# Kernel optimization log

Hardware: AMD Instinct MI355X
Metric: run time of the kernel (lower is better)

Reference implementation:

```python
import jax, jax.numpy as jnp
import numpy as np

EMBED_DIM = 1024
NUM_HEADS = 16
HEAD_DIM = EMBED_DIM // NUM_HEADS
BOARD = 32
SEQ = BOARD * BOARD
BATCH = 16


def setup_inputs() -> dict:
    key = jax.random.key(0)
    ks = jax.random.split(key, 6)
    x = jax.random.normal(ks[0], (BATCH, SEQ, EMBED_DIM), dtype=jnp.float32)
    scale = 1.0 / np.sqrt(EMBED_DIM)
    Wq = jax.random.normal(ks[1], (EMBED_DIM, EMBED_DIM), dtype=jnp.float32) * scale
    Wk = jax.random.normal(ks[2], (EMBED_DIM, EMBED_DIM), dtype=jnp.float32) * scale
    Wv = jax.random.normal(ks[3], (EMBED_DIM, EMBED_DIM), dtype=jnp.float32) * scale
    Wo = jax.random.normal(ks[4], (EMBED_DIM, EMBED_DIM), dtype=jnp.float32) * scale
    rel_bias = jax.random.normal(ks[5], (NUM_HEADS, 2 * BOARD - 1), dtype=jnp.float32)
    return {"x": x, "Wq": Wq, "Wk": Wk, "Wv": Wv, "Wo": Wo, "rel_bias": rel_bias}


def _rel_indices():
    # coords of the flattened H*W grid
    idx = jnp.arange(SEQ)
    rows = idx // BOARD
    cols = idx % BOARD
    offset = BOARD - 1
    rel_x = cols[None, :] - cols[:, None] + offset  # [S, S]
    rel_y = rows[None, :] - rows[:, None] + offset  # [S, S]
    return rel_x, rel_y


def reference(x, Wq, Wk, Wv, Wo, rel_bias):
    B, S, E = x.shape
    H, D = NUM_HEADS, HEAD_DIM
    # projections (Linear with bias=False: x @ W.T; weights here stored as [E, E] applied as x @ W)
    q = (x @ Wq).reshape(B, S, H, D).transpose(0, 2, 1, 3)  # [B,H,S,D]
    k = (x @ Wk).reshape(B, S, H, D).transpose(0, 2, 1, 3)
    v = (x @ Wv).reshape(B, S, H, D).transpose(0, 2, 1, 3)
    scores = jnp.einsum('bhqd,bhkd->bhqk', q, k) / jnp.sqrt(jnp.float32(D))
    rel_x, rel_y = _rel_indices()
    bias = rel_bias[:, rel_x] + rel_bias[:, rel_y]  # [H, S, S]
    scores = scores + bias[None]
    attn = jax.nn.softmax(scores, axis=-1)
    out = jnp.einsum('bhqk,bhkd->bhqd', attn, v)
    out = out.transpose(0, 2, 1, 3).reshape(B, S, E)
    return out @ Wo
```

## Files before the change

### kernel.cpp

```cpp
#include <hip/hip_runtime.h>

#define SEQ   1024
#define EMBED 1024
#define NH    16
#define HD    64
#define NB    16

typedef float facc4 __attribute__((ext_vector_type(4)));
typedef float facc16 __attribute__((ext_vector_type(16)));
typedef short frag8 __attribute__((ext_vector_type(8)));
typedef short sv4 __attribute__((ext_vector_type(4)));

__device__ __forceinline__ unsigned short f2bf(float f) {
  union { float f; unsigned int u; } c; c.f = f;
  unsigned int u = c.u;
  u += 0x7FFFu + ((u >> 16) & 1u);
  return (unsigned short)(u >> 16);
}

__device__ __forceinline__ unsigned int pk_bf16(float lo, float hi) {
  unsigned int r;
  asm("v_cvt_pk_bf16_f32 %0, %1, %2" : "=v"(r) : "v"(lo), "v"(hi));
  return r;
}

__device__ __forceinline__ void gl_lds16(const void* g, void* l) {
  __builtin_amdgcn_global_load_lds(
      (const __attribute__((address_space(1))) unsigned int*)g,
      (__attribute__((address_space(3))) unsigned int*)l, 16, 0, 0);
}

__global__ __launch_bounds__(256) void convert_x_kernel(
    const float* __restrict__ x, unsigned short* __restrict__ xb, int n8) {
  int stride = gridDim.x * blockDim.x;
  for (int i = blockIdx.x * blockDim.x + threadIdx.x; i < n8; i += stride) {
    const float4* src = (const float4*)(x + (size_t)i * 8);
    float4 v0 = src[0], v1 = src[1];
    frag8 o;
    o[0] = f2bf(v0.x); o[1] = f2bf(v0.y); o[2] = f2bf(v0.z); o[3] = f2bf(v0.w);
    o[4] = f2bf(v1.x); o[5] = f2bf(v1.y); o[6] = f2bf(v1.z); o[7] = f2bf(v1.w);
    *(frag8*)(xb + (size_t)i * 8) = o;
  }
}

__global__ __launch_bounds__(256) void transpose_w_kernel(
    const float* W0, const float* W1, const float* W2, const float* W3,
    unsigned short* T0, unsigned short* T1, unsigned short* T2, unsigned short* T3) {
  __shared__ float tw[64][65];
  const float* W; unsigned short* T;
  switch (blockIdx.z) {
    case 0: W = W0; T = T0; break;
    case 1: W = W1; T = T1; break;
    case 2: W = W2; T = T2; break;
    default: W = W3; T = T3; break;
  }
  int k0 = blockIdx.y * 64, n0 = blockIdx.x * 64;
  int t = threadIdx.x;
#pragma unroll
  for (int rep = 0; rep < 4; ++rep) {
    int c = rep * 256 + t;
    int row = c >> 4, ch = c & 15;
    float4 v = *(const float4*)(W + (size_t)(k0 + row) * 1024 + n0 + ch * 4);
    tw[row][ch * 4 + 0] = v.x; tw[row][ch * 4 + 1] = v.y;
    tw[row][ch * 4 + 2] = v.z; tw[row][ch * 4 + 3] = v.w;
  }
  __syncthreads();
#pragma unroll
  for (int rep = 0; rep < 2; ++rep) {
    int c = rep * 256 + t;
    int nrow = c >> 3, ch = c & 7;
    frag8 o;
#pragma unroll
    for (int i = 0; i < 8; ++i) o[i] = (short)f2bf(tw[ch * 8 + i][nrow]);
    *(frag8*)(T + (size_t)(n0 + nrow) * 1024 + k0 + ch * 8) = o;
  }
}

template <int MODE>
__global__ __launch_bounds__(512, 2) void gemm256(
    const unsigned short* __restrict__ A, const unsigned short* __restrict__ Bt,
    unsigned short* __restrict__ qo, unsigned short* __restrict__ ko,
    unsigned short* __restrict__ vto, float* __restrict__ fo, int N) {
  __shared__ unsigned short a_s[2][256 * 64];
  __shared__ unsigned short b_s[2][256 * 64];
  const int tid = threadIdx.x;
  const int w = tid >> 6, l = tid & 63;
  const int l15 = l & 15, l4 = l >> 4;
  const int wr = w >> 2, wc = w & 3;

  const int bid = blockIdx.x;
  const int xcd = bid & 7, j = bid >> 3;
  const int mt = xcd * 8 + (j & 7), nt = j >> 3;
  const int m0 = mt << 8, n0 = nt << 8;

  const int ldrow = l >> 3;
  const int swz8 = ((l & 7) ^ (ldrow & 7)) << 3;
  const unsigned short* Ab = A + (size_t)m0 * 1024;
  const unsigned short* Bb = Bt + (size_t)n0 * 1024;

  facc4 acc[8][4];
#pragma unroll
  for (int mi = 0; mi < 8; ++mi)
#pragma unroll
    for (int nj = 0; nj < 4; ++nj)
#pragma unroll
      for (int r = 0; r < 4; ++r) acc[mi][nj][r] = 0.f;

  auto STAGE_A = [&](int buf, int half, int kt) {
#pragma unroll
    for (int i = 0; i < 2; ++i) {
      const int c = (w << 1) + i;
      const int rb = (half << 7) + (c << 3);
      gl_lds16(Ab + (size_t)kt * 64 + (size_t)(rb + ldrow) * 1024 + swz8,
               &a_s[buf][rb << 6]);
    }
  };
  auto STAGE_B = [&](int buf, int half, int kt) {
#pragma unroll
    for (int i = 0; i < 2; ++i) {
      const int c = (w << 1) + i;
      const int rb = (half << 7) + (c << 3);
      gl_lds16(Bb + (size_t)kt * 64 + (size_t)(rb + ldrow) * 1024 + swz8,
               &b_s[buf][rb << 6]);
    }
  };

  STAGE_A(0, 0, 0); STAGE_A(0, 1, 0);
  STAGE_B(0, 0, 0); STAGE_B(0, 1, 0);
  STAGE_B(1, 0, 1); STAGE_B(1, 1, 1);
  asm volatile("s_waitcnt vmcnt(4)" ::: "memory");
  __builtin_amdgcn_s_barrier();

  const int rowA = (wr << 7) + l15;
  const int rowB = (wc << 6) + l15;

  frag8 aq[4][2], bq0[2][2], bq1[2][2];

  for (int u = 0; u < 16; ++u) {
    const int p = u & 1;
    const unsigned short* ap = a_s[p];
    const unsigned short* bp = b_s[p];

#pragma unroll
    for (int mi = 0; mi < 4; ++mi) {
      const int r = rowA + (mi << 4);
#pragma unroll
      for (int ks = 0; ks < 2; ++ks)
        aq[mi][ks] = *(const frag8*)(ap + (r << 6) + ((((ks << 2) | l4) ^ (r & 7)) << 3));
    }
#pragma unroll
    for (int nj = 0; nj < 2; ++nj) {
      const int r = rowB + (nj << 4);
#pragma unroll
      for (int ks = 0; ks < 2; ++ks)
        bq0[nj][ks] = *(const frag8*)(bp + (r << 6) + ((((ks << 2) | l4) ^ (r & 7)) << 3));
    }
    if (u + 1 < 16) STAGE_A(p ^ 1, 0, u + 1);
    asm volatile("s_waitcnt lgkmcnt(8)" ::: "memory");
    __builtin_amdgcn_s_barrier();
    asm volatile("s_waitcnt lgkmcnt(0)" ::: "memory");
    __builtin_amdgcn_s_setprio(1);
#pragma unroll
    for (int ks = 0; ks < 2; ++ks)
#pragma unroll
      for (int mi = 0; mi < 4; ++mi)
#pragma unroll
        for (int nj = 0; nj < 2; ++nj)
          acc[mi][nj] = __builtin_amdgcn_mfma_f32_16x16x32_bf16(
              aq[mi][ks], bq0[nj][ks], acc[mi][nj], 0, 0, 0);
    __builtin_amdgcn_s_setprio(0);
    __builtin_amdgcn_s_barrier();

#pragma unroll
    for (int nj = 0; nj < 2; ++nj) {
      const int r = rowB + ((nj + 2) << 4);
#pragma unroll
      for (int ks = 0; ks < 2; ++ks)
        bq1[nj][ks] = *(const frag8*)(bp + (r << 6) + ((((ks << 2) | l4) ^ (r & 7)) << 3));
    }
    if (u + 1 < 16) STAGE_A(p ^ 1, 1, u + 1);
    __builtin_amdgcn_s_barrier();
    asm volatile("s_waitcnt lgkmcnt(0)" ::: "memory");
    __builtin_amdgcn_s_setprio(1);
#pragma unroll
    for (int ks = 0; ks < 2; ++ks)
#pragma unroll
      for (int mi = 0; mi < 4; ++mi)
#pragma unroll
        for (int nj = 0; nj < 2; ++nj)
          acc[mi][nj + 2] = __builtin_amdgcn_mfma_f32_16x16x32_bf16(
              aq[mi][ks], bq1[nj][ks], acc[mi][nj + 2], 0, 0, 0);
    __builtin_amdgcn_s_setprio(0);
    __builtin_amdgcn_s_barrier();

#pragma unroll
    for (int mi = 0; mi < 4; ++mi) {
      const int r = rowA + ((mi + 4) << 4);
#pragma unroll
      for (int ks = 0; ks < 2; ++ks)
        aq[mi][ks] = *(const frag8*)(ap + (r << 6) + ((((ks << 2) | l4) ^ (r & 7)) << 3));
    }
    if (u + 2 < 16) STAGE_B(p, 0, u + 2);
    __builtin_amdgcn_s_barrier();
    asm volatile("s_waitcnt lgkmcnt(0)" ::: "memory");
    __builtin_amdgcn_s_setprio(1);
#pragma unroll
    for (int ks = 0; ks < 2; ++ks)
#pragma unroll
      for (int mi = 0; mi < 4; ++mi)
#pragma unroll
        for (int nj = 0; nj < 2; ++nj)
          acc[mi + 4][nj + 2] = __builtin_amdgcn_mfma_f32_16x16x32_bf16(
              aq[mi][ks], bq1[nj][ks], acc[mi + 4][nj + 2], 0, 0, 0);
    __builtin_amdgcn_s_setprio(0);
    __builtin_amdgcn_s_barrier();

    if (u + 2 < 16) STAGE_B(p, 1, u + 2);
    __builtin_amdgcn_s_barrier();
    __builtin_amdgcn_s_setprio(1);
#pragma unroll
    for (int ks = 0; ks < 2; ++ks)
#pragma unroll
      for (int mi = 0; mi < 4; ++mi)
#pragma unroll
        for (int nj = 0; nj < 2; ++nj)
          acc[mi + 4][nj] = __builtin_amdgcn_mfma_f32_16x16x32_bf16(
              aq[mi][ks], bq0[nj][ks], acc[mi + 4][nj], 0, 0, 0);
    __builtin_amdgcn_s_setprio(0);
    if (u < 14)       asm volatile("s_waitcnt vmcnt(4)" ::: "memory");
    else if (u == 14) asm volatile("s_waitcnt vmcnt(0)" ::: "memory");
    if (u < 15) __builtin_amdgcn_s_barrier();
  }

  const int m_base = m0 + (wr << 7);
  if (MODE == 0) {
    const int bb16 = (m_base >> 10) << 4;
#pragma unroll
    for (int nj = 0; nj < 4; ++nj) {
      const int n = n0 + (wc << 6) + (nj << 4) + l15;
      const int proj = n >> 10, rem = n & 1023;
      const int h = rem >> 6, d = rem & 63;
      const size_t bh16 = ((size_t)(bb16 + h)) << 16;
      if (proj == 2) {
#pragma unroll
        for (int mi = 0; mi < 8; ++mi) {
          const int s0 = (m_base + (mi << 4) + (l4 << 2)) & 1023;
          sv4 pv;
#pragma unroll
          for (int rr = 0; rr < 4; ++rr) pv[rr] = (short)f2bf(acc[mi][nj][rr]);
          *(sv4*)(vto + bh16 + ((size_t)d << 10) + s0) = pv;
        }
      } else {
        unsigned short* dst = (proj == 0) ? qo : ko;
#pragma unroll
        for (int mi = 0; mi < 8; ++mi)
#pragma unroll
          for (int rr = 0; rr < 4; ++rr) {
            const int s = (m_base + (mi << 4) + (l4 << 2) + rr) & 1023;
            dst[bh16 + (size_t)s * 64 + d] = f2bf(acc[mi][nj][rr]);
          }
      }
    }
  } else {
#pragma unroll
    for (int nj = 0; nj < 4; ++nj) {
      const int n = n0 + (wc << 6) + (nj << 4) + l15;
#pragma unroll
      for (int mi = 0; mi < 8; ++mi)
#pragma unroll
        for (int rr = 0; rr < 4; ++rr) {
          const int m = m_base + (mi << 4) + (l4 << 2) + rr;
          fo[(size_t)m * N + n] = acc[mi][nj][rr];
        }
    }
  }
}

__global__ __launch_bounds__(256, 4) void attn_kernel(
    const unsigned short* __restrict__ q, const unsigned short* __restrict__ k,
    const unsigned short* __restrict__ vt, const float* __restrict__ rel_bias,
    unsigned short* __restrict__ ao) {
  __shared__ unsigned short smem[16384];
  __shared__ float rb_s[63];
  unsigned short* k_s = smem;
  unsigned short* v_s = smem + 8192;

  const int bid = blockIdx.x;
  const int xcd = bid & 7, jj = bid >> 3;
  const int bh = xcd * 32 + (jj >> 3), qt = jj & 7;
  const int b = bh >> 4, h = bh & 15;
  const int t = threadIdx.x, w = t >> 6, l = t & 63;
  const int l31 = l & 31, hi = l >> 5;

  if (t < 63) rb_s[t] = rel_bias[h * 63 + t] * 1.44269504f;

  const unsigned short* qg = q + (size_t)bh * (SEQ * 64);
  const unsigned short* kg = k + (size_t)bh * (SEQ * 64);
  const unsigned short* vg = vt + (size_t)bh * (64 * SEQ);

  const int q0 = qt * 128 + w * 32;
  const int qr = q0 >> 5;

  frag8 qf[4];
#pragma unroll
  for (int s = 0; s < 4; ++s)
    qf[s] = *(const frag8*)(qg + (size_t)(q0 + l31) * 64 + s * 16 + hi * 8);

  auto STAGE = [&](int buf, int kt) {
#pragma unroll
    for (int i = 0; i < 2; ++i) {
      const int c = i * 256 + t;
      const int row = c >> 3, ch = c & 7;
      const int sw = (ch ^ (row & 7)) << 3;
      const int base = ((i * 256 + w * 64) << 3) + buf * 4096;
      gl_lds16(kg + (size_t)(kt * 64 + row) * 64 + sw, k_s + base);
      gl_lds16(vg + (size_t)row * SEQ + kt * 64 + sw, v_s + base);
    }
  };
  STAGE(0, 0);

  asm volatile("s_waitcnt lgkmcnt(0)" ::: "memory");
  __builtin_amdgcn_s_barrier();

  float bx[16];
#pragma unroll
  for (int r = 0; r < 16; ++r) {
    const int kc = (r & 3) + 8 * (r >> 2) + 4 * hi;
    bx[r] = rb_s[kc - l31 + 31];
  }

  float m_run = -1e30f, lsum = 0.f;
  facc16 o0, o1;
#pragma unroll
  for (int i = 0; i < 16; ++i) { o0[i] = 0.f; o1[i] = 0.f; }

  const float C1 = 0.125f * 1.44269504f;

  for (int kt = 0; kt < 16; ++kt) {
    const int p = kt & 1;
    if (kt < 15) {
      STAGE(p ^ 1, kt + 1);
      asm volatile("s_waitcnt vmcnt(4)" ::: "memory");
    } else {
      asm volatile("s_waitcnt vmcnt(0)" ::: "memory");
    }
    __builtin_amdgcn_s_barrier();

    const char* kp = (const char*)(k_s + p * 4096);
    const char* vp = (const char*)(v_s + p * 4096);

    facc16 sa[2];
    __builtin_amdgcn_s_setprio(1);
#pragma unroll
    for (int st = 0; st < 2; ++st) {
      facc16 z;
#pragma unroll
      for (int i = 0; i < 16; ++i) z[i] = 0.f;
#pragma unroll
      for (int s = 0; s < 4; ++s) {
        const int row = st * 32 + l31;
        const int byte_off = row * 128 + (((s * 2 + hi) ^ (row & 7)) << 4);
        frag8 kf = *(const frag8*)(kp + byte_off);
        z = __builtin_amdgcn_mfma_f32_32x32x16_bf16(kf, qf[s], z, 0, 0, 0);
      }
      sa[st] = z;
    }
    __builtin_amdgcn_s_setprio(0);

    const float by0 = rb_s[kt * 2 + 0 - qr + 31];
    const float by1 = rb_s[kt * 2 + 1 - qr + 31];
    float sc0[16], sc1[16];
#pragma unroll
    for (int r = 0; r < 16; ++r) {
      sc0[r] = __builtin_fmaf(sa[0][r], C1, bx[r]);
      sc1[r] = __builtin_fmaf(sa[1][r], C1, bx[r]);
    }
    float m0 = sc0[0], m1 = sc1[0];
#pragma unroll
    for (int r = 1; r < 16; ++r) { m0 = fmaxf(m0, sc0[r]); m1 = fmaxf(m1, sc1[r]); }
    float tm = fmaxf(m0 + by0, m1 + by1);
    tm = fmaxf(tm, __shfl_xor(tm, 32));
    if (!__all(tm <= m_run + 8.f)) {
      const float mn = fmaxf(m_run, tm);
      const float corr = __builtin_amdgcn_exp2f(m_run - mn);
      lsum *= corr;
#pragma unroll
      for (int i = 0; i < 16; ++i) { o0[i] *= corr; o1[i] *= corr; }
      m_run = mn;
    }
    const float mb0 = m_run - by0, mb1 = m_run - by1;
    float p0[16], p1[16];
    float ps = 0.f;
#pragma unroll
    for (int r = 0; r < 16; ++r) {
      p0[r] = __builtin_amdgcn_exp2f(sc0[r] - mb0);
      p1[r] = __builtin_amdgcn_exp2f(sc1[r] - mb1);
      ps += p0[r] + p1[r];
    }
    ps += __shfl_xor(ps, 32);
    lsum += ps;

    unsigned int fw[4][4];
#pragma unroll
    for (int ks = 0; ks < 4; ++ks) {
      const float* pp = (ks < 2) ? p0 : p1;
      const int R0 = (ks & 1) * 8;
      const int R1 = R0 + 4;
      const unsigned int w00 = pk_bf16(pp[R0 + 0], pp[R0 + 1]);
      const unsigned int w01 = pk_bf16(pp[R0 + 2], pp[R0 + 3]);
      const unsigned int w10 = pk_bf16(pp[R1 + 0], pp[R1 + 1]);
      const unsigned int w11 = pk_bf16(pp[R1 + 2], pp[R1 + 3]);
      const unsigned int s0 = hi ? w00 : w10;
      const unsigned int s1 = hi ? w01 : w11;
      const unsigned int r0 = __shfl_xor((int)s0, 32);
      const unsigned int r1 = __shfl_xor((int)s1, 32);
      fw[ks][0] = hi ? r0 : w00;
      fw[ks][1] = hi ? r1 : w01;
      fw[ks][2] = hi ? w10 : r0;
      fw[ks][3] = hi ? w11 : r1;
    }

    __builtin_amdgcn_s_setprio(1);
#pragma unroll
    for (int ks = 0; ks < 4; ++ks) {
      frag8 pb;
      {
        union { unsigned int u[4]; frag8 f; } cv;
        cv.u[0] = fw[ks][0]; cv.u[1] = fw[ks][1];
        cv.u[2] = fw[ks][2]; cv.u[3] = fw[ks][3];
        pb = cv.f;
      }
      {
        const int row = l31;
        const int byte_off = row * 128 + (((ks * 2 + hi) ^ (row & 7)) << 4);
        frag8 vf = *(const frag8*)(vp + byte_off);
        o0 = __builtin_amdgcn_mfma_f32_32x32x16_bf16(vf, pb, o0, 0, 0, 0);
      }
      {
        const int row = 32 + l31;
        const int byte_off = row * 128 + (((ks * 2 + hi) ^ (row & 7)) << 4);
        frag8 vf = *(const frag8*)(vp + byte_off);
        o1 = __builtin_amdgcn_mfma_f32_32x32x16_bf16(vf, pb, o1, 0, 0, 0);
      }
    }
    __builtin_amdgcn_s_setprio(0);

    asm volatile("s_waitcnt lgkmcnt(0)" ::: "memory");
    __builtin_amdgcn_s_barrier();
  }

  const float inv = __builtin_amdgcn_rcpf(lsum);
  unsigned short (*os)[72] = (unsigned short (*)[72])(smem + w * (32 * 72));
#pragma unroll
  for (int dt = 0; dt < 2; ++dt) {
#pragma unroll
    for (int r = 0; r < 16; r += 2) {
      const int d = (r & 3) + 8 * (r >> 2) + 4 * hi + 32 * dt;
      const float e0 = (dt ? o1[r] : o0[r]) * inv;
      const float e1 = (dt ? o1[r + 1] : o0[r + 1]) * inv;
      *(unsigned int*)&os[l31][d] = pk_bf16(e0, e1);
    }
  }
  asm volatile("s_waitcnt lgkmcnt(0)" ::: "memory");
#pragma unroll
  for (int i = 0; i < 4; ++i) {
    const int c = i * 64 + l;
    const int qrow = c >> 3, ch = c & 7;
    frag8 ov = *(const frag8*)(&os[qrow][ch * 8]);
    *(frag8*)(ao + ((size_t)(b * SEQ + q0 + qrow) * EMBED + h * 64 + ch * 8)) = ov;
  }
}

extern "C" void kernel_launch(void* const* d_in, const int* in_sizes, int n_in,
                              void* d_out, int out_size, void* d_ws, size_t ws_size,
                              hipStream_t stream) {
  (void)in_sizes; (void)n_in; (void)out_size; (void)ws_size;
  const float* x  = (const float*)d_in[0];
  const float* Wq = (const float*)d_in[1];
  const float* Wk = (const float*)d_in[2];
  const float* Wv = (const float*)d_in[3];
  const float* Wo = (const float*)d_in[4];
  const float* rb = (const float*)d_in[5];
  float* out = (float*)d_out;

  unsigned short* xb  = (unsigned short*)d_ws;
  unsigned short* wtq = xb + 16777216;
  unsigned short* wtk = wtq + 1048576;
  unsigned short* wtv = wtk + 1048576;
  unsigned short* wto = wtv + 1048576;
  unsigned short* qb  = wto + 1048576;
  unsigned short* kb  = qb + 16777216;
  unsigned short* aob = kb + 16777216;
  unsigned short* vtb = aob + 16777216;

  convert_x_kernel<<<4096, 256, 0, stream>>>(x, xb, 16777216 / 8);
  transpose_w_kernel<<<dim3(16, 16, 4), 256, 0, stream>>>(
      Wq, Wk, Wv, Wo, wtq, wtk, wtv, wto);
  gemm256<0><<<768, 512, 0, stream>>>(
      xb, wtq, qb, kb, vtb, nullptr, 3072);
  attn_kernel<<<2048, 256, 0, stream>>>(qb, kb, vtb, rb, aob);
  gemm256<1><<<256, 512, 0, stream>>>(
      aob, wto, nullptr, nullptr, nullptr, out, 1024);
}
```

Baseline: 302.9 us.

## Restructure GEMM main loop to defer last MFMA quadrant into next iteration

Reworks the software pipeline of the projection GEMM: B is now prefetched only one tile ahead instead of two, and the fourth MFMA quadrant of each K-step is deferred into the next iteration, overlapping it with the next tile's A-fragment loads and global staging. A separate fragment register set (a1/b0 kept live) enables this, and the trailing quadrant is issued after the loop. The goal is to hide LDS read and barrier latency behind MFMA work. In exchange it raises register pressure and shortens the global prefetch distance.

```diff
diff --git a/kernel.cpp b/kernel.cpp
--- a/kernel.cpp
+++ b/kernel.cpp
@@ -127,17 +127,16 @@
 
   STAGE_A(0, 0, 0); STAGE_A(0, 1, 0);
   STAGE_B(0, 0, 0); STAGE_B(0, 1, 0);
-  STAGE_B(1, 0, 1); STAGE_B(1, 1, 1);
   asm volatile("s_waitcnt vmcnt(4)" ::: "memory");
   __builtin_amdgcn_s_barrier();
 
   const int rowA = (wr << 7) + l15;
   const int rowB = (wc << 6) + l15;
 
-  frag8 aq[4][2], bq0[2][2], bq1[2][2];
-
-  for (int u = 0; u < 16; ++u) {
-    const int p = u & 1;
+  frag8 a0[4][2], a1[4][2], b0[2][2], b1[2][2];
+
+  for (int t = 0; t < 16; ++t) {
+    const int p = t & 1, q = p ^ 1;
     const unsigned short* ap = a_s[p];
     const unsigned short* bp = b_s[p];
 
@@ -146,17 +145,38 @@
       const int r = rowA + (mi << 4);
 #pragma unroll
       for (int ks = 0; ks < 2; ++ks)
-        aq[mi][ks] = *(const frag8*)(ap + (r << 6) + ((((ks << 2) | l4) ^ (r & 7)) << 3));
-    }
+        a0[mi][ks] = *(const frag8*)(ap + (r << 6) + ((((ks << 2) | l4) ^ (r & 7)) << 3));
+    }
+    if (t < 15) {
+      STAGE_A(q, 0, t + 1);
+      asm volatile("s_waitcnt vmcnt(2)" ::: "memory");
+    } else {
+      asm volatile("s_waitcnt vmcnt(0)" ::: "memory");
+    }
+    __builtin_amdgcn_s_barrier();
+    asm volatile("s_waitcnt lgkmcnt(0)" ::: "memory");
+    if (t > 0) {
+      __builtin_amdgcn_s_setprio(1);
+#pragma unroll
+      for (int ks = 0; ks < 2; ++ks)
+#pragma unroll
+        for (int mi = 0; mi < 4; ++mi)
+#pragma unroll
+          for (int nj = 0; nj < 2; ++nj)
+            acc[mi + 4][nj] = __builtin_amdgcn_mfma_f32_16x16x32_bf16(
+                a1[mi][ks], b0[nj][ks], acc[mi + 4][nj], 0, 0, 0);
+      __builtin_amdgcn_s_setprio(0);
+    }
+    __builtin_amdgcn_s_barrier();
+
 #pragma unroll
     for (int nj = 0; nj < 2; ++nj) {
       const int r = rowB + (nj << 4);
 #pragma unroll
       for (int ks = 0; ks < 2; ++ks)
-        bq0[nj][ks] = *(const frag8*)(bp + (r << 6) + ((((ks << 2) | l4) ^ (r & 7)) << 3));
-    }
-    if (u + 1 < 16) STAGE_A(p ^ 1, 0, u + 1);
-    asm volatile("s_waitcnt lgkmcnt(8)" ::: "memory");
+        b0[nj][ks] = *(const frag8*)(bp + (r << 6) + ((((ks << 2) | l4) ^ (r & 7)) << 3));
+    }
+    if (t < 15) STAGE_A(q, 1, t + 1);
     __builtin_amdgcn_s_barrier();
     asm volatile("s_waitcnt lgkmcnt(0)" ::: "memory");
     __builtin_amdgcn_s_setprio(1);
@@ -167,7 +187,7 @@
 #pragma unroll
         for (int nj = 0; nj < 2; ++nj)
           acc[mi][nj] = __builtin_amdgcn_mfma_f32_16x16x32_bf16(
-              aq[mi][ks], bq0[nj][ks], acc[mi][nj], 0, 0, 0);
+              a0[mi][ks], b0[nj][ks], acc[mi][nj], 0, 0, 0);
     __builtin_amdgcn_s_setprio(0);
     __builtin_amdgcn_s_barrier();
 
@@ -176,9 +196,9 @@
       const int r = rowB + ((nj + 2) << 4);
 #pragma unroll
       for (int ks = 0; ks < 2; ++ks)
-        bq1[nj][ks] = *(const frag8*)(bp + (r << 6) + ((((ks << 2) | l4) ^ (r & 7)) << 3));
-    }
-    if (u + 1 < 16) STAGE_A(p ^ 1, 1, u + 1);
+        b1[nj][ks] = *(const frag8*)(bp + (r << 6) + ((((ks << 2) | l4) ^ (r & 7)) << 3));
+    }
+    if (t < 15) STAGE_B(q, 0, t + 1);
     __builtin_amdgcn_s_barrier();
     asm volatile("s_waitcnt lgkmcnt(0)" ::: "memory");
     __builtin_amdgcn_s_setprio(1);
@@ -189,7 +209,7 @@
 #pragma unroll
         for (int nj = 0; nj < 2; ++nj)
           acc[mi][nj + 2] = __builtin_amdgcn_mfma_f32_16x16x32_bf16(
-              aq[mi][ks], bq1[nj][ks], acc[mi][nj + 2], 0, 0, 0);
+              a0[mi][ks], b1[nj][ks], acc[mi][nj + 2], 0, 0, 0);
     __builtin_amdgcn_s_setprio(0);
     __builtin_amdgcn_s_barrier();
 
@@ -198,9 +218,12 @@
       const int r = rowA + ((mi + 4) << 4);
 #pragma unroll
       for (int ks = 0; ks < 2; ++ks)
-        aq[mi][ks] = *(const frag8*)(ap + (r << 6) + ((((ks << 2) | l4) ^ (r & 7)) << 3));
-    }
-    if (u + 2 < 16) STAGE_B(p, 0, u + 2);
+        a1[mi][ks] = *(const frag8*)(ap + (r << 6) + ((((ks << 2) | l4) ^ (r & 7)) << 3));
+    }
+    if (t < 15) {
+      STAGE_B(q, 1, t + 1);
+      asm volatile("s_waitcnt vmcnt(4)" ::: "memory");
+    }
     __builtin_amdgcn_s_barrier();
     asm volatile("s_waitcnt lgkmcnt(0)" ::: "memory");
     __builtin_amdgcn_s_setprio(1);
@@ -211,26 +234,21 @@
 #pragma unroll
         for (int nj = 0; nj < 2; ++nj)
           acc[mi + 4][nj + 2] = __builtin_amdgcn_mfma_f32_16x16x32_bf16(
-              aq[mi][ks], bq1[nj][ks], acc[mi + 4][nj + 2], 0, 0, 0);
+              a1[mi][ks], b1[nj][ks], acc[mi + 4][nj + 2], 0, 0, 0);
     __builtin_amdgcn_s_setprio(0);
-    __builtin_amdgcn_s_barrier();
-
-    if (u + 2 < 16) STAGE_B(p, 1, u + 2);
-    __builtin_amdgcn_s_barrier();
-    __builtin_amdgcn_s_setprio(1);
-#pragma unroll
-    for (int ks = 0; ks < 2; ++ks)
-#pragma unroll
-      for (int mi = 0; mi < 4; ++mi)
-#pragma unroll
-        for (int nj = 0; nj < 2; ++nj)
-          acc[mi + 4][nj] = __builtin_amdgcn_mfma_f32_16x16x32_bf16(
-              aq[mi][ks], bq0[nj][ks], acc[mi + 4][nj], 0, 0, 0);
-    __builtin_amdgcn_s_setprio(0);
-    if (u < 14)       asm volatile("s_waitcnt vmcnt(4)" ::: "memory");
-    else if (u == 14) asm volatile("s_waitcnt vmcnt(0)" ::: "memory");
-    if (u < 15) __builtin_amdgcn_s_barrier();
-  }
+    if (t < 15) __builtin_amdgcn_s_barrier();
+  }
+
+  __builtin_amdgcn_s_setprio(1);
+#pragma unroll
+  for (int ks = 0; ks < 2; ++ks)
+#pragma unroll
+    for (int mi = 0; mi < 4; ++mi)
+#pragma unroll
+      for (int nj = 0; nj < 2; ++nj)
+        acc[mi + 4][nj] = __builtin_amdgcn_mfma_f32_16x16x32_bf16(
+            a1[mi][ks], b0[nj][ks], acc[mi + 4][nj], 0, 0, 0);
+  __builtin_amdgcn_s_setprio(0);
 
   const int m_base = m0 + (wr << 7);
   if (MODE == 0) {
```

Measured after the change: 282.5 us. 6.7% less time.
